# Performance work log

Measured on AMD Instinct MI355X. Metric: run time of the kernel, lower is better.

Reference implementation:

```python
import jax, jax.numpy as jnp
import numpy as np

C = 1.0            # curvature
KEEP_RATIO = 0.5
MIN_NORM = 1e-15
BALL_EPS = 4e-3    # hgcn PoincareBall projection epsilon


def _norm(x):
    return jnp.maximum(jnp.linalg.norm(x, axis=-1, keepdims=True), MIN_NORM)


def proj(x, c):
    n = _norm(x)
    maxnorm = (1.0 - BALL_EPS) / jnp.sqrt(c)
    return jnp.where(n > maxnorm, x / n * maxnorm, x)


def expmap0(u, c):
    sc = jnp.sqrt(c)
    n = _norm(u)
    return jnp.tanh(sc * n) * u / (sc * n)


def logmap0(p, c):
    # proj_tan0 is identity on the Poincare ball
    sc = jnp.sqrt(c)
    n = _norm(p)
    t = jnp.clip(sc * n, -1.0 + 1e-7, 1.0 - 1e-7)
    return jnp.arctanh(t) * p / (sc * n)


def mobius_add(x, y, c):
    x2 = jnp.sum(x * x, -1, keepdims=True)
    y2 = jnp.sum(y * y, -1, keepdims=True)
    xy = jnp.sum(x * y, -1, keepdims=True)
    num = (1 + 2 * c * xy + c * y2) * x + (1 - c * x2) * y
    den = 1 + 2 * c * xy + c * c * x2 * y2
    return num / jnp.maximum(den, MIN_NORM)


def setup_inputs() -> dict:
    key = jax.random.key(0)
    N, D, E = 100000, 512, 3200000
    k0, k1, k2, k3, k4 = jax.random.split(key, 5)
    # points must lie inside the Poincare ball: scale down then project
    x = 0.01 * jax.random.normal(k0, (N, D), jnp.float32)
    x = proj(x, C)
    weight = jax.random.normal(k1, (D, 1), jnp.float32) * float(np.sqrt(6.0 / (D + 1)))  # xavier-ish
    bias = jnp.zeros((1,), jnp.float32)
    adj_vals = jax.random.uniform(k2, (E,), jnp.float32)
    edge_rows = jax.random.randint(k3, (E,), 0, N, jnp.int32)
    edge_cols = jax.random.randint(k4, (E,), 0, N, jnp.int32)
    return {
        "input_feature": x,
        "adj_vals": adj_vals,
        "weight": weight,
        "bias": bias,
        "w1": jnp.float32(0.5),
        "b": jnp.float32(0.0),
        "edge_rows": edge_rows,
        "edge_cols": edge_cols,
    }


def reference(input_feature, adj_vals, weight, bias, w1, b, edge_rows, edge_cols):
    N = input_feature.shape[0]
    # --- HypGraphConvolution(input_dim -> 1) ---
    x_tan = logmap0(input_feature, C)              # [N, D]
    support = x_tan @ weight                       # [N, 1]
    hyp_bias = proj(expmap0(bias[None, :], C), C)  # [1, 1]
    support = proj(mobius_add(support, hyp_bias, C), C)
    # sparse adj @ support via gather + segment_sum
    gathered = adj_vals[:, None] * support[edge_cols]            # [E, 1]
    agg = jax.ops.segment_sum(gathered, edge_rows, num_segments=N)  # [N, 1]
    score = proj(expmap0(agg, C), C)
    # --- pooling head ---
    attn = jnp.tanh(score[:, 0])                   # squeeze -> [N]
    norm = jnp.sqrt(C) * jnp.linalg.norm(input_feature, axis=-1)  # manifold.normalize
    attn = w1 * attn + (1 - w1) * (1 - norm) + b
    k = int(KEEP_RATIO * N)
    _, idx = jax.lax.top_k(attn, k)
    idx = jnp.sort(idx)                            # boolean mask preserves node order
    x_euc = logmap0(input_feature, C)              # logmap0 then proj_tan0 (identity)
    hidden = x_euc[idx] * attn[idx][:, None]       # [k, D]
    return hidden, attn
```

## Files before the change

### kernel.cpp

```cpp
#include <hip/hip_runtime.h>
#include <stdint.h>

#define CHUNK 3072
#define BROWS 256
#define CAP   12288
#define SUB   8
#define SUBLEN (CAP / SUB)

__global__ __launch_bounds__(256) void rowstats(
    const float* __restrict__ x, const float* __restrict__ w,
    const float* __restrict__ bias, const float* __restrict__ w1p,
    const float* __restrict__ bp,
    float* __restrict__ support, float* __restrict__ coef,
    double* __restrict__ base,
    uint32_t* __restrict__ hist1, uint32_t* __restrict__ hist2,
    uint32_t* __restrict__ M, int N)
{
    if (blockIdx.x < 256) {
        int z = blockIdx.x * 256 + threadIdx.x;
        hist1[z] = 0u; hist2[z] = 0u;
    } else if (blockIdx.x == 256 && threadIdx.x < 8) M[threadIdx.x] = 0u;

    int wv = threadIdx.x >> 6, lane = threadIdx.x & 63;
    int row = blockIdx.x * 4 + wv;
    if (row >= N) return;
    const float4* xr = (const float4*)(x + (size_t)row * 512);
    const float4* wr = (const float4*)(w);
    float dot = 0.f, ss = 0.f;
#pragma unroll
    for (int it = 0; it < 2; it++) {
        float4 xv = xr[lane + it * 64];
        float4 wv4 = wr[lane + it * 64];
        dot += xv.x * wv4.x + xv.y * wv4.y + xv.z * wv4.z + xv.w * wv4.w;
        ss  += xv.x * xv.x + xv.y * xv.y + xv.z * xv.z + xv.w * xv.w;
    }
    for (int off = 32; off; off >>= 1) {
        dot += __shfl_xor(dot, off);
        ss  += __shfl_xor(ss, off);
    }
    if (lane == 0) {
        double n = sqrt((double)ss); if (n < 1e-15) n = 1e-15;
        double t = n; const double lim = 1.0 - 1e-7; if (t > lim) t = lim;
        double cf = atanh(t) / n;
        double s = cf * (double)dot;
        const double maxn = 0.996;
        double b0 = (double)bias[0];
        double r;
        if (b0 == 0.0) {
            r = s;
        } else {
            double nb = fabs(b0); if (nb < 1e-15) nb = 1e-15;
            double hb = tanh(nb) * b0 / nb;
            double nh = fabs(hb); if (nh < 1e-15) nh = 1e-15;
            if (nh > maxn) hb = hb / nh * maxn;
            double x2 = s * s, y2 = hb * hb, xy = s * hb;
            double num = (1.0 + 2.0 * xy + y2) * s + (1.0 - x2) * hb;
            double den = 1.0 + 2.0 * xy + x2 * y2;
            if (den < 1e-15) den = 1e-15;
            r = num / den;
        }
        double nr = fabs(r); if (nr < 1e-15) nr = 1e-15;
        if (nr > maxn) r = r / nr * maxn;
        support[row] = (float)r;
        coef[row] = (float)cf;
        double w1 = (double)w1p[0];
        double bb = (double)bp[0];
        base[row] = (1.0 - w1) * (1.0 - n) + bb;
    }
}

__device__ __forceinline__ float attn_math(double a, double base_i, double w1)
{
    double na = fabs(a); if (na < 1e-15) na = 1e-15;
    double sc_ = tanh(na) * a / na;
    const double maxn = 0.996;
    double ns = fabs(sc_); if (ns < 1e-15) ns = 1e-15;
    if (ns > maxn) sc_ = sc_ / ns * maxn;
    return (float)(w1 * tanh(sc_) + base_i);
}

__device__ __forceinline__ uint32_t key_of(float af)
{
    union { float f; uint32_t u; } cv; cv.f = af;
    return cv.u ^ ((cv.u >> 31) ? 0xFFFFFFFFu : 0x80000000u);
}

__global__ __launch_bounds__(256) void spmv(
    const int* __restrict__ rows, const int* __restrict__ cols,
    const float* __restrict__ adj, const float* __restrict__ support,
    unsigned long long* __restrict__ agg, int E)
{
    int e = blockIdx.x * 256 + threadIdx.x;
    if (e >= E) return;
    double p = (double)adj[e] * (double)support[cols[e]];
    long long f = llrint(p * 1073741824.0);
    atomicAdd(&agg[rows[e]], (unsigned long long)f);
}

__global__ __launch_bounds__(256) void attn_from_agg(
    const unsigned long long* __restrict__ agg, const double* __restrict__ base,
    const float* __restrict__ w1p,
    float* __restrict__ attn, uint32_t* __restrict__ keys,
    uint32_t* __restrict__ hist1, float* __restrict__ attn_out, int N)
{
    int i = blockIdx.x * 256 + threadIdx.x;
    if (i >= N) return;
    double a = (double)(long long)agg[i] * (1.0 / 1073741824.0);
    float af = attn_math(a, base[i], (double)w1p[0]);
    attn[i] = af; attn_out[i] = af;
    uint32_t key = key_of(af);
    keys[i] = key;
    atomicAdd(&hist1[key >> 16], 1u);
}

__global__ __launch_bounds__(256) void edge_hist(
    const int* __restrict__ rows, uint32_t* __restrict__ P,
    int E, int nbuk, int nchunks)
{
    __shared__ uint32_t h[512];
    int b = blockIdx.x;
    for (int q = threadIdx.x; q < 512; q += 256) h[q] = 0u;
    __syncthreads();
    int s = b * CHUNK, e_end = min(E, s + CHUNK);
    for (int i = s + threadIdx.x; i < e_end; i += 256)
        atomicAdd(&h[((uint32_t)rows[i]) >> 8], 1u);
    __syncthreads();
    for (int q = threadIdx.x; q < nbuk; q += 256)
        P[(size_t)q * nchunks + b] = h[q];
}

__global__ __launch_bounds__(64) void scan_parts(
    uint32_t* __restrict__ P, uint32_t* __restrict__ tot, int nchunks)
{
    int q = blockIdx.x, lane = threadIdx.x;
    uint32_t* row = P + (size_t)q * nchunks;
    uint32_t run = 0;
    for (int base = 0; base < nchunks; base += 64) {
        int idx = base + lane;
        uint32_t v = (idx < nchunks) ? row[idx] : 0u;
        uint32_t inc = v;
        for (int off = 1; off < 64; off <<= 1) {
            uint32_t t = __shfl_up(inc, off);
            if (lane >= off) inc += t;
        }
        if (idx < nchunks) row[idx] = run + inc - v;
        run += __shfl(inc, 63);
    }
    if (lane == 0) tot[q] = (run > CAP) ? CAP : run;
}

__global__ __launch_bounds__(256) void edge_sort_scatter(
    const int* __restrict__ rows, const int* __restrict__ cols,
    const float* __restrict__ adj, const float* __restrict__ support,
    const uint32_t* __restrict__ P,
    int* __restrict__ prod, uint8_t* __restrict__ rowlo,
    int E, int nbuk, int nchunks)
{
    __shared__ uint32_t lcnt[512], lofs[512], gbase[512], sc[512];
    __shared__ int      lpi[CHUNK];
    __shared__ uint16_t lq[CHUNK];
    __shared__ uint8_t  lrl[CHUNK];
    int b = blockIdx.x, t = threadIdx.x;
    int s = b * CHUNK;
    int n = min(CHUNK, E - s);
    if (n <= 0) return;
    for (int q = t; q < 512; q += 256) lcnt[q] = 0u;
    __syncthreads();
    for (int i = t; i < n; i += 256)
        atomicAdd(&lcnt[((uint32_t)rows[s + i]) >> 8], 1u);
    __syncthreads();
    uint32_t a0 = lcnt[t], a1 = lcnt[t + 256];
    sc[t] = a0; sc[t + 256] = a1;
    __syncthreads();
    for (int off = 1; off < 512; off <<= 1) {
        uint32_t u0 = (t >= off) ? sc[t - off] : 0u;
        uint32_t u1 = ((t + 256) >= off) ? sc[t + 256 - off] : 0u;
        __syncthreads();
        sc[t] += u0; sc[t + 256] += u1;
        __syncthreads();
    }
    lofs[t] = sc[t] - a0;
    lofs[t + 256] = sc[t + 256] - a1;
    for (int q = t; q < 512; q += 256) {
        gbase[q] = (q < nbuk) ? ((uint32_t)q * CAP + P[(size_t)q * nchunks + b]) : 0u;
        lcnt[q] = 0u;
    }
    __syncthreads();
    for (int i = t; i < n; i += 256) {
        uint32_t r = (uint32_t)rows[s + i];
        uint32_t q = r >> 8;
        double p = (double)adj[s + i] * (double)support[cols[s + i]];
        int pi = (int)llrint(p * 1073741824.0);
        uint32_t rank = atomicAdd(&lcnt[q], 1u);
        uint32_t slot = lofs[q] + rank;
        lpi[slot] = pi;
        lq[slot]  = (uint16_t)q;
        lrl[slot] = (uint8_t)(r & 255u);
    }
    __syncthreads();
    for (int i = t; i < n; i += 256) {
        uint32_t q = lq[i];
        uint32_t gpos = gbase[q] + ((uint32_t)i - lofs[q]);
        if (gpos < (q + 1u) * CAP) {
            prod[gpos]  = lpi[i];
            rowlo[gpos] = lrl[i];
        }
    }
}

__global__ __launch_bounds__(256) void reduce_part(
    const int* __restrict__ prod, const uint8_t* __restrict__ rowlo,
    const uint32_t* __restrict__ tot,
    unsigned long long* __restrict__ agg_part)
{
    __shared__ unsigned long long acc[BROWS];
    int blk = blockIdx.x, t = threadIdx.x;
    int q = blk >> 3, s = blk & (SUB - 1);
    acc[t] = 0ull;
    __syncthreads();
    uint32_t t0 = tot[q];
    uint32_t lo = (uint32_t)s * SUBLEN;
    uint32_t hi = t0 < lo + SUBLEN ? t0 : lo + SUBLEN;
    uint32_t base = (uint32_t)q * CAP;
    for (uint32_t i = lo + t; i < hi; i += 256)
        atomicAdd(&acc[rowlo[base + i]], (unsigned long long)(long long)prod[base + i]);
    __syncthreads();
    agg_part[((size_t)blk << 8) | t] = acc[t];
}

__global__ __launch_bounds__(256) void attn_kernel2(
    const unsigned long long* __restrict__ agg_part, const double* __restrict__ base,
    const float* __restrict__ w1p,
    float* __restrict__ attn, uint32_t* __restrict__ keys,
    uint32_t* __restrict__ hist1, float* __restrict__ attn_out, int N)
{
    int i = blockIdx.x * 256 + threadIdx.x;
    if (i >= N) return;
    int q = i >> 8, r = i & 255;
    long long a64 = 0;
#pragma unroll
    for (int s = 0; s < SUB; s++)
        a64 += (long long)agg_part[(((size_t)q * SUB + s) << 8) | r];
    double a = (double)a64 * (1.0 / 1073741824.0);
    float af = attn_math(a, base[i], (double)w1p[0]);
    attn[i] = af; attn_out[i] = af;
    uint32_t key = key_of(af);
    keys[i] = key;
    atomicAdd(&hist1[key >> 16], 1u);
}

__global__ __launch_bounds__(1024) void select_bucket(
    const uint32_t* __restrict__ hist, uint32_t* M, int mode, uint32_t k)
{
    __shared__ uint32_t lds[1024];
    int t = threadIdx.x;
    uint32_t ktarget = (mode == 0) ? k : (k - M[1]);
    uint32_t csum = 0;
    for (int j = 0; j < 64; j++) csum += hist[t * 64 + j];
    lds[t] = csum;
    __syncthreads();
    for (int off = 1; off < 1024; off <<= 1) {
        uint32_t v = (t + off < 1024) ? lds[t + off] : 0u;
        __syncthreads();
        lds[t] += v;
        __syncthreads();
    }
    uint32_t run = (t + 1 < 1024) ? lds[t + 1] : 0u;
    for (int j = 63; j >= 0; j--) {
        uint32_t c = hist[t * 64 + j];
        uint32_t nr = run + c;
        if (nr >= ktarget && run < ktarget) {
            if (mode == 0) { M[0] = (uint32_t)(t * 64 + j); M[1] = run; }
            else           { M[2] = (M[0] << 16) | (uint32_t)(t * 64 + j);
                             M[3] = ktarget - run; }
        }
        run = nr;
    }
}

__global__ __launch_bounds__(256) void hist_low(
    const uint32_t* __restrict__ keys, const uint32_t* __restrict__ M,
    uint32_t* __restrict__ hist2, int N)
{
    int i = blockIdx.x * 256 + threadIdx.x;
    if (i >= N) return;
    uint32_t key = keys[i];
    if ((key >> 16) == M[0]) atomicAdd(&hist2[key & 0xFFFFu], 1u);
}


__global__ __launch_bounds__(1024) void select_write2(
    const uint32_t* __restrict__ keys, const uint32_t* __restrict__ M,
    uint32_t* __restrict__ sel, int N)
{
    __shared__ uint32_t red_s[16], red_t[16];
    uint32_t tau = M[2], need = M[3];
    int t = threadIdx.x, lane = t & 63, wv = t >> 6;
    uint32_t start = (uint32_t)blockIdx.x * 1024u;
    uint32_t cs = 0, ct = 0;
    for (uint32_t i = t; i < start; i += 1024) {
        uint32_t kk = keys[i];
        cs += (kk > tau);
        ct += (kk == tau);
    }
    for (int off = 32; off; off >>= 1) {
        cs += __shfl_xor(cs, off);
        ct += __shfl_xor(ct, off);
    }
    if (lane == 0) { red_s[wv] = cs; red_t[wv] = ct; }
    __syncthreads();
    uint32_t gs0 = 0, gt0 = 0;
    for (int q = 0; q < 16; q++) { gs0 += red_s[q]; gt0 += red_t[q]; }
    __syncthreads();
    uint32_t i = start + (uint32_t)t;
    uint32_t kk = (i < (uint32_t)N) ? keys[i] : 0u;
    uint32_t f = (i < (uint32_t)N) && (kk > tau);
    uint32_t g = (i < (uint32_t)N) && (kk == tau);
    uint32_t is = f, it = g;
    for (int off = 1; off < 64; off <<= 1) {
        uint32_t vs = __shfl_up(is, off);
        uint32_t vt = __shfl_up(it, off);
        if (lane >= off) { is += vs; it += vt; }
    }
    if (lane == 63) { red_s[wv] = is; red_t[wv] = it; }
    __syncthreads();
    uint32_t wos = 0, wot = 0;
    for (int q = 0; q < wv; q++) { wos += red_s[q]; wot += red_t[q]; }
    uint32_t gs = gs0 + wos + is - f;
    uint32_t gt = gt0 + wot + it - g;
    if (f)                   sel[gs + (gt < need ? gt : need)] = i;
    else if (g && gt < need) sel[gs + gt] = i;
}

__global__ __launch_bounds__(256) void write_hidden(
    const float* __restrict__ x, const uint32_t* __restrict__ sel,
    const float* __restrict__ attn, const float* __restrict__ coef,
    float* __restrict__ out, int K)
{
    int wv = threadIdx.x >> 6, lane = threadIdx.x & 63;
    int p = blockIdx.x * 4 + wv;
    if (p >= K) return;
    uint32_t i = sel[p];
    float s = attn[i] * coef[i];
    const float4* xr = (const float4*)(x + (size_t)i * 512);
    float4* orow = (float4*)(out + (size_t)p * 512);
#pragma unroll
    for (int it = 0; it < 2; it++) {
        float4 v = xr[lane + it * 64];
        float4 o;
        o.x = v.x * s; o.y = v.y * s; o.z = v.z * s; o.w = v.w * s;
        orow[lane + it * 64] = o;
    }
}

extern "C" void kernel_launch(void* const* d_in, const int* in_sizes, int n_in,
                              void* d_out, int out_size, void* d_ws, size_t ws_size,
                              hipStream_t stream)
{
    const float* x    = (const float*)d_in[0];
    const float* adj  = (const float*)d_in[1];
    const float* w    = (const float*)d_in[2];
    const float* bias = (const float*)d_in[3];
    const float* w1p  = (const float*)d_in[4];
    const float* bp   = (const float*)d_in[5];
    const int* erow = (const int*)d_in[6];
    const int* ecol = (const int*)d_in[7];

    int D = in_sizes[2];
    int N = in_sizes[0] / D;
    int E = in_sizes[1];
    int K = N / 2;

    char* ws = (char*)d_ws;
    float*   support = (float*)(ws);
    float*   coef    = (float*)(ws + (1 << 20));
    double*  base    = (double*)(ws + (2 << 20));
    float*   attn    = (float*)(ws + (3 << 20));
    uint32_t* keys   = (uint32_t*)(ws + (4 << 20));
    uint32_t* hist1  = (uint32_t*)(ws + (5 << 20));
    uint32_t* hist2  = (uint32_t*)(ws + (5 << 20) + (256 << 10));
    uint32_t* M      = (uint32_t*)(ws + (5 << 20) + (512 << 10));
    uint32_t* sel    = (uint32_t*)(ws + (6 << 20));
    uint32_t* P      = (uint32_t*)(ws + (7 << 20));
    uint32_t* tot    = (uint32_t*)(ws + (9 << 20));
    int*      prod   = (int*)(ws + (12 << 20));
    uint8_t*  rowlo  = (uint8_t*)(ws + (32 << 20));
    unsigned long long* agg_part = (unsigned long long*)(ws + (37 << 20));
    unsigned long long* agg = (unsigned long long*)(ws + (44 << 20));

    float* hidden_out = (float*)d_out;
    float* attn_out   = (float*)d_out + (size_t)K * D;

    int nbuk = (N + BROWS - 1) / BROWS;
    int nchunks = (E + CHUNK - 1) / CHUNK;
    bool fast = (ws_size >= (size_t)(48 << 20)) && (nbuk <= 512);

    rowstats<<<(N + 3) / 4, 256, 0, stream>>>(x, w, bias, w1p, bp,
                                              support, coef, base, hist1, hist2, M, N);

    if (fast) {
        edge_hist<<<nchunks, 256, 0, stream>>>(erow, P, E, nbuk, nchunks);
        scan_parts<<<nbuk, 64, 0, stream>>>(P, tot, nchunks);
        edge_sort_scatter<<<nchunks, 256, 0, stream>>>(erow, ecol, adj, support, P,
                                                       prod, rowlo, E, nbuk, nchunks);
        reduce_part<<<nbuk * SUB, 256, 0, stream>>>(prod, rowlo, tot, agg_part);
        attn_kernel2<<<(N + 255) / 256, 256, 0, stream>>>(agg_part, base, w1p,
                                                          attn, keys, hist1, attn_out, N);
    } else {
        hipMemsetAsync(agg, 0, (size_t)N * 8, stream);
        spmv<<<(E + 255) / 256, 256, 0, stream>>>(erow, ecol, adj, support, agg, E);
        attn_from_agg<<<(N + 255) / 256, 256, 0, stream>>>(agg, base, w1p,
                                                           attn, keys, hist1, attn_out, N);
    }

    select_bucket<<<1, 1024, 0, stream>>>(hist1, M, 0, (uint32_t)K);
    hist_low<<<(N + 255) / 256, 256, 0, stream>>>(keys, M, hist2, N);
    select_bucket<<<1, 1024, 0, stream>>>(hist2, M, 1, (uint32_t)K);
    int nb = (N + 1023) / 1024;
    select_write2<<<nb, 1024, 0, stream>>>(keys, M, sel, N);
    write_hidden<<<(K + 3) / 4, 256, 0, stream>>>(x, sel, attn, coef, hidden_out, K);
}
```

Baseline: 371.5 us.

## Replace edge histogram and scan passes with atomic bucket reservation

Drops the separate edge_hist and scan_parts kernels. Each chunk in edge_sort_scatter now reserves its slot range in every row bucket with one global atomicAdd on a per-bucket cursor, zeroed in rowstats. This removes a full read of edge_rows and two kernel launches. In exchange, edge order inside each bucket is no longer deterministic, but the integer fixed-point accumulation still gives exact sums, and overflow past CAP is still clamped.

```diff
diff --git a/kernel.cpp b/kernel.cpp
--- a/kernel.cpp
+++ b/kernel.cpp
@@ -14,12 +14,18 @@
     float* __restrict__ support, float* __restrict__ coef,
     double* __restrict__ base,
     uint32_t* __restrict__ hist1, uint32_t* __restrict__ hist2,
-    uint32_t* __restrict__ M, int N)
+    uint32_t* __restrict__ M, uint32_t* __restrict__ cur, int N)
 {
     if (blockIdx.x < 256) {
         int z = blockIdx.x * 256 + threadIdx.x;
         hist1[z] = 0u; hist2[z] = 0u;
-    } else if (blockIdx.x == 256 && threadIdx.x < 8) M[threadIdx.x] = 0u;
+    } else if (blockIdx.x == 256) {
+        if (threadIdx.x < 8) M[threadIdx.x] = 0u;
+    } else if (blockIdx.x == 257) {
+        cur[threadIdx.x] = 0u;
+    } else if (blockIdx.x == 258) {
+        cur[256 + threadIdx.x] = 0u;
+    }
 
     int wv = threadIdx.x >> 6, lane = threadIdx.x & 63;
     int row = blockIdx.x * 4 + wv;
@@ -113,48 +119,11 @@
     atomicAdd(&hist1[key >> 16], 1u);
 }
 
-__global__ __launch_bounds__(256) void edge_hist(
-    const int* __restrict__ rows, uint32_t* __restrict__ P,
-    int E, int nbuk, int nchunks)
-{
-    __shared__ uint32_t h[512];
-    int b = blockIdx.x;
-    for (int q = threadIdx.x; q < 512; q += 256) h[q] = 0u;
-    __syncthreads();
-    int s = b * CHUNK, e_end = min(E, s + CHUNK);
-    for (int i = s + threadIdx.x; i < e_end; i += 256)
-        atomicAdd(&h[((uint32_t)rows[i]) >> 8], 1u);
-    __syncthreads();
-    for (int q = threadIdx.x; q < nbuk; q += 256)
-        P[(size_t)q * nchunks + b] = h[q];
-}
-
-__global__ __launch_bounds__(64) void scan_parts(
-    uint32_t* __restrict__ P, uint32_t* __restrict__ tot, int nchunks)
-{
-    int q = blockIdx.x, lane = threadIdx.x;
-    uint32_t* row = P + (size_t)q * nchunks;
-    uint32_t run = 0;
-    for (int base = 0; base < nchunks; base += 64) {
-        int idx = base + lane;
-        uint32_t v = (idx < nchunks) ? row[idx] : 0u;
-        uint32_t inc = v;
-        for (int off = 1; off < 64; off <<= 1) {
-            uint32_t t = __shfl_up(inc, off);
-            if (lane >= off) inc += t;
-        }
-        if (idx < nchunks) row[idx] = run + inc - v;
-        run += __shfl(inc, 63);
-    }
-    if (lane == 0) tot[q] = (run > CAP) ? CAP : run;
-}
-
 __global__ __launch_bounds__(256) void edge_sort_scatter(
     const int* __restrict__ rows, const int* __restrict__ cols,
     const float* __restrict__ adj, const float* __restrict__ support,
-    const uint32_t* __restrict__ P,
-    int* __restrict__ prod, uint8_t* __restrict__ rowlo,
-    int E, int nbuk, int nchunks)
+    uint32_t* __restrict__ cur,
+    int* __restrict__ prod, uint8_t* __restrict__ rowlo, int E, int nbuk)
 {
     __shared__ uint32_t lcnt[512], lofs[512], gbase[512], sc[512];
     __shared__ int      lpi[CHUNK];
@@ -182,7 +151,10 @@
     lofs[t] = sc[t] - a0;
     lofs[t + 256] = sc[t + 256] - a1;
     for (int q = t; q < 512; q += 256) {
-        gbase[q] = (q < nbuk) ? ((uint32_t)q * CAP + P[(size_t)q * nchunks + b]) : 0u;
+        uint32_t cnt = (q == t) ? a0 : a1;
+        uint32_t rsv = 0u;
+        if (q < nbuk && cnt > 0) rsv = atomicAdd(&cur[q], cnt);
+        gbase[q] = (uint32_t)q * CAP + rsv;
         lcnt[q] = 0u;
     }
     __syncthreads();
@@ -210,7 +182,7 @@
 
 __global__ __launch_bounds__(256) void reduce_part(
     const int* __restrict__ prod, const uint8_t* __restrict__ rowlo,
-    const uint32_t* __restrict__ tot,
+    const uint32_t* __restrict__ cur,
     unsigned long long* __restrict__ agg_part)
 {
     __shared__ unsigned long long acc[BROWS];
@@ -218,7 +190,7 @@
     int q = blk >> 3, s = blk & (SUB - 1);
     acc[t] = 0ull;
     __syncthreads();
-    uint32_t t0 = tot[q];
+    uint32_t t0 = cur[q]; if (t0 > CAP) t0 = CAP;
     uint32_t lo = (uint32_t)s * SUBLEN;
     uint32_t hi = t0 < lo + SUBLEN ? t0 : lo + SUBLEN;
     uint32_t base = (uint32_t)q * CAP;
@@ -288,7 +260,6 @@
     if ((key >> 16) == M[0]) atomicAdd(&hist2[key & 0xFFFFu], 1u);
 }
 
-
 __global__ __launch_bounds__(1024) void select_write2(
     const uint32_t* __restrict__ keys, const uint32_t* __restrict__ M,
     uint32_t* __restrict__ sel, int N)
@@ -381,8 +352,7 @@
     uint32_t* hist2  = (uint32_t*)(ws + (5 << 20) + (256 << 10));
     uint32_t* M      = (uint32_t*)(ws + (5 << 20) + (512 << 10));
     uint32_t* sel    = (uint32_t*)(ws + (6 << 20));
-    uint32_t* P      = (uint32_t*)(ws + (7 << 20));
-    uint32_t* tot    = (uint32_t*)(ws + (9 << 20));
+    uint32_t* cur    = (uint32_t*)(ws + (9 << 20));
     int*      prod   = (int*)(ws + (12 << 20));
     uint8_t*  rowlo  = (uint8_t*)(ws + (32 << 20));
     unsigned long long* agg_part = (unsigned long long*)(ws + (37 << 20));
@@ -396,14 +366,12 @@
     bool fast = (ws_size >= (size_t)(48 << 20)) && (nbuk <= 512);
 
     rowstats<<<(N + 3) / 4, 256, 0, stream>>>(x, w, bias, w1p, bp,
-                                              support, coef, base, hist1, hist2, M, N);
+                                              support, coef, base, hist1, hist2, M, cur, N);
 
     if (fast) {
-        edge_hist<<<nchunks, 256, 0, stream>>>(erow, P, E, nbuk, nchunks);
-        scan_parts<<<nbuk, 64, 0, stream>>>(P, tot, nchunks);
-        edge_sort_scatter<<<nchunks, 256, 0, stream>>>(erow, ecol, adj, support, P,
-                                                       prod, rowlo, E, nbuk, nchunks);
-        reduce_part<<<nbuk * SUB, 256, 0, stream>>>(prod, rowlo, tot, agg_part);
+        edge_sort_scatter<<<nchunks, 256, 0, stream>>>(erow, ecol, adj, support, cur,
+                                                       prod, rowlo, E, nbuk);
+        reduce_part<<<nbuk * SUB, 256, 0, stream>>>(prod, rowlo, cur, agg_part);
         attn_kernel2<<<(N + 255) / 256, 256, 0, stream>>>(agg_part, base, w1p,
                                                           attn, keys, hist1, attn_out, N);
     } else {
```

Measured after the change: 379.2 us. +2.1%, slower.
